# Optimization experiments

Hardware: AMD Instinct MI355X
Metric: run time of the kernel (lower is better)

Reference implementation:

```python
import jax, jax.numpy as jnp
import numpy as np

E = 100000          # number of edges
IN_FEATS = 256      # in_edge_feats
HIDDEN = 128        # hidden_size
K = 16              # neighbors per edge (uniform-degree rendering of ragged lists)


def setup_inputs() -> dict:
    key = jax.random.key(0)
    k1, k2, k3, k4 = jax.random.split(key, 4)
    edge_feats = jax.random.normal(k1, (E, IN_FEATS), dtype=jnp.float32)
    neighbors = jax.random.randint(k2, (E, K), 0, E, dtype=jnp.int32)
    # Linear params (torch Linear: y = x @ W^T + b; here W stored as [in, out])
    W = jax.random.normal(k3, (IN_FEATS, HIDDEN), dtype=jnp.float32) / np.sqrt(IN_FEATS)
    b = jax.random.normal(k4, (HIDDEN,), dtype=jnp.float32) * 0.01
    return {"edge_feats": edge_feats, "neighbors": neighbors, "W": W, "b": b}


def reference(edge_feats, neighbors, W, b):
    # Dense linear transform of all edge features: [E, H]
    t = edge_feats @ W + b
    # Gather each edge's K neighbor transformed features and sum: [E, K, H] -> [E, H]
    nbr_sum = jnp.take(t, neighbors, axis=0).sum(axis=1)
    # agg[i] = t[i] + sum_{n in neighbors[i]} t[n]
    return t + nbr_sum
```

## Files before the change

kernel.cpp:

```cpp
#include <hip/hip_runtime.h>
#include <hip/hip_bf16.h>
#include <stdint.h>

#define E_EDGES 100000
#define IN_F    256
#define HID     128
#define KNB     16
#define NCHUNK  ((E_EDGES + 63) / 64)
#define GEMM_GRID 512

typedef short bf16x8 __attribute__((ext_vector_type(8)));
typedef float f32x4  __attribute__((ext_vector_type(4)));

__device__ __forceinline__ unsigned short f2bf(float f) {
    union { float f; unsigned u; } v; v.f = f;
    unsigned u = v.u;
    u += 0x7fffu + ((u >> 16) & 1u);
    return (unsigned short)(u >> 16);
}

__global__ void conv_w_kernel(const float* __restrict__ W, unsigned short* __restrict__ Wtf) {
    int d = blockIdx.x * 256 + threadIdx.x;
    int f = d >> 6, L = d & 63;
    int k0 = f >> 3, ct = f & 7, quad = L >> 4, l15 = L & 15;
    int n  = ct * 16 + l15;
    int kb = (k0 * 4 + quad) * 8;
    const float* wp = W + (size_t)kb * HID + n;
    unsigned short h[8];
    #pragma unroll
    for (int j = 0; j < 8; ++j) h[j] = f2bf(wp[(size_t)j * HID]);
    uint4 o;
    o.x = (unsigned)h[0] | ((unsigned)h[1] << 16);
    o.y = (unsigned)h[2] | ((unsigned)h[3] << 16);
    o.z = (unsigned)h[4] | ((unsigned)h[5] << 16);
    o.w = (unsigned)h[6] | ((unsigned)h[7] << 16);
    *(uint4*)(Wtf + (size_t)d * 8) = o;
}

__launch_bounds__(256, 2)
__global__ void gemm_t_kernel(const float* __restrict__ A,
                              const unsigned short* __restrict__ Wtf,
                              const float* __restrict__ bias,
                              unsigned short* __restrict__ T) {
    __shared__ unsigned short Bs[32768];
    const int tid  = threadIdx.x;
    const int wave = tid >> 6;
    const int lane = tid & 63;
    const int l15  = lane & 15;
    const int quad = lane >> 4;

    #pragma unroll
    for (int it = 0; it < 16; ++it) {
        int d = it * 256 + tid;
        *(uint4*)(Bs + (size_t)d * 8) = *(const uint4*)(Wtf + (size_t)d * 8);
    }

    float bv[8];
    #pragma unroll
    for (int ct = 0; ct < 8; ++ct) bv[ct] = bias[ct * 16 + l15];

    __syncthreads();

    for (int c = blockIdx.x; c < NCHUNK; c += GEMM_GRID) {
        const int rowbase = c * 64 + wave * 16;
        int arow = rowbase + l15;
        if (arow >= E_EDGES) arow = E_EDGES - 1;

        const float* ap = A + (size_t)arow * IN_F + quad * 8;
        float4 af32[16];
        #pragma unroll
        for (int k0 = 0; k0 < 8; ++k0) {
            af32[2 * k0]     = *(const float4*)(ap + k0 * 32);
            af32[2 * k0 + 1] = *(const float4*)(ap + k0 * 32 + 4);
        }

        bf16x8 apre[8];
        #pragma unroll
        for (int k0 = 0; k0 < 8; ++k0) {
            float4 lo = af32[2 * k0], hi = af32[2 * k0 + 1];
            bf16x8 f;
            f[0] = (short)f2bf(lo.x); f[1] = (short)f2bf(lo.y);
            f[2] = (short)f2bf(lo.z); f[3] = (short)f2bf(lo.w);
            f[4] = (short)f2bf(hi.x); f[5] = (short)f2bf(hi.y);
            f[6] = (short)f2bf(hi.z); f[7] = (short)f2bf(hi.w);
            apre[k0] = f;
        }

        f32x4 acc[8] = {};
        #pragma unroll
        for (int k0 = 0; k0 < 8; ++k0) {
            #pragma unroll
            for (int ct = 0; ct < 8; ++ct) {
                bf16x8 bf = *(const bf16x8*)(Bs + ((size_t)((k0 * 8 + ct) * 64 + lane)) * 8);
                acc[ct] = __builtin_amdgcn_mfma_f32_16x16x32_bf16(apre[k0], bf, acc[ct], 0, 0, 0);
            }
        }

        #pragma unroll
        for (int ct = 0; ct < 8; ++ct) {
            const int col = ct * 16 + l15;
            #pragma unroll
            for (int i = 0; i < 4; ++i) {
                const int row = rowbase + quad * 4 + i;
                if (row < E_EDGES)
                    T[(size_t)row * HID + col] = f2bf(acc[ct][i] + bv[ct]);
            }
        }
    }
}

__launch_bounds__(256)
__global__ void gather_sum_kernel(const unsigned short* __restrict__ T,
                                  const int* __restrict__ nbr,
                                  float* __restrict__ out) {
    __shared__ int sidx[256];
    const int tid   = threadIdx.x;
    const int edge0 = blockIdx.x * 16;
    sidx[tid] = nbr[(size_t)edge0 * KNB + tid];
    __syncthreads();

    const int el   = tid >> 4;
    const int lane = tid & 15;
    const int edge = edge0 + el;

    const unsigned short* tb = T + (size_t)lane * 8;
    uint4 v[17];
    v[0] = *(const uint4*)(tb + (size_t)edge * HID);
    #pragma unroll
    for (int k = 0; k < KNB; ++k)
        v[k + 1] = *(const uint4*)(tb + (size_t)sidx[el * KNB + k] * HID);
    __builtin_amdgcn_sched_barrier(0);

    float acc[8] = {};
    #pragma unroll
    for (int k = 0; k < 17; ++k) {
        unsigned w[4] = { v[k].x, v[k].y, v[k].z, v[k].w };
        union { unsigned u; float f; } c;
        #pragma unroll
        for (int j = 0; j < 4; ++j) {
            c.u = w[j] << 16;          acc[2 * j]     += c.f;
            c.u = w[j] & 0xffff0000u;  acc[2 * j + 1] += c.f;
        }
    }

    float* op = out + (size_t)edge * HID + lane * 8;
    float4 o0 = { acc[0], acc[1], acc[2], acc[3] };
    float4 o1 = { acc[4], acc[5], acc[6], acc[7] };
    *(float4*)op       = o0;
    *(float4*)(op + 4) = o1;
}

extern "C" void kernel_launch(void* const* d_in, const int* in_sizes, int n_in,
                              void* d_out, int out_size, void* d_ws, size_t ws_size,
                              hipStream_t stream) {
    const float* edge_feats = (const float*)d_in[0];
    const int*   neighbors  = (const int*)d_in[1];
    const float* W          = (const float*)d_in[2];
    const float* b          = (const float*)d_in[3];
    float*       out        = (float*)d_out;

    unsigned short* Wtf = (unsigned short*)d_ws;
    unsigned short* T   = (unsigned short*)d_ws + (size_t)IN_F * HID;

    conv_w_kernel<<<16, 256, 0, stream>>>(W, Wtf);
    gemm_t_kernel<<<GEMM_GRID, 256, 0, stream>>>(edge_feats, Wtf, b, T);
    gather_sum_kernel<<<E_EDGES / 16, 256, 0, stream>>>(T, neighbors, out);
}
```

Baseline: 263.4 us.

## Prefetch next A chunk and transpose MFMA to vectorize T stores

Result: faster. 231.7 us (-12.0%).

```diff
diff --git a/kernel.cpp b/kernel.cpp
--- a/kernel.cpp
+++ b/kernel.cpp
@@ -49,31 +49,31 @@
     const int l15  = lane & 15;
     const int quad = lane >> 4;
 
+    int c = blockIdx.x;
+    int arow = c * 64 + wave * 16 + l15;
+    if (arow >= E_EDGES) arow = E_EDGES - 1;
+    const float* ap = A + (size_t)arow * IN_F + quad * 8;
+    float4 af32[16];
+    #pragma unroll
+    for (int k0 = 0; k0 < 8; ++k0) {
+        af32[2 * k0]     = *(const float4*)(ap + k0 * 32);
+        af32[2 * k0 + 1] = *(const float4*)(ap + k0 * 32 + 4);
+    }
+
     #pragma unroll
     for (int it = 0; it < 16; ++it) {
         int d = it * 256 + tid;
         *(uint4*)(Bs + (size_t)d * 8) = *(const uint4*)(Wtf + (size_t)d * 8);
     }
 
-    float bv[8];
+    float4 bv4[8];
     #pragma unroll
-    for (int ct = 0; ct < 8; ++ct) bv[ct] = bias[ct * 16 + l15];
+    for (int ct = 0; ct < 8; ++ct)
+        bv4[ct] = *(const float4*)(bias + ct * 16 + quad * 4);
 
     __syncthreads();
 
-    for (int c = blockIdx.x; c < NCHUNK; c += GEMM_GRID) {
-        const int rowbase = c * 64 + wave * 16;
-        int arow = rowbase + l15;
-        if (arow >= E_EDGES) arow = E_EDGES - 1;
-
-        const float* ap = A + (size_t)arow * IN_F + quad * 8;
-        float4 af32[16];
-        #pragma unroll
-        for (int k0 = 0; k0 < 8; ++k0) {
-            af32[2 * k0]     = *(const float4*)(ap + k0 * 32);
-            af32[2 * k0 + 1] = *(const float4*)(ap + k0 * 32 + 4);
-        }
-
+    for (; c < NCHUNK; c += GEMM_GRID) {
         bf16x8 apre[8];
         #pragma unroll
         for (int k0 = 0; k0 < 8; ++k0) {
@@ -86,24 +86,42 @@
             apre[k0] = f;
         }
 
+        {
+            int cn = c + GEMM_GRID;
+            int arow2 = cn * 64 + wave * 16 + l15;
+            if (arow2 >= E_EDGES) arow2 = E_EDGES - 1;
+            const float* ap2 = A + (size_t)arow2 * IN_F + quad * 8;
+            #pragma unroll
+            for (int k0 = 0; k0 < 8; ++k0) {
+                af32[2 * k0]     = *(const float4*)(ap2 + k0 * 32);
+                af32[2 * k0 + 1] = *(const float4*)(ap2 + k0 * 32 + 4);
+            }
+        }
+        __builtin_amdgcn_sched_barrier(0);
+
         f32x4 acc[8] = {};
         #pragma unroll
         for (int k0 = 0; k0 < 8; ++k0) {
             #pragma unroll
             for (int ct = 0; ct < 8; ++ct) {
                 bf16x8 bf = *(const bf16x8*)(Bs + ((size_t)((k0 * 8 + ct) * 64 + lane)) * 8);
-                acc[ct] = __builtin_amdgcn_mfma_f32_16x16x32_bf16(apre[k0], bf, acc[ct], 0, 0, 0);
+                acc[ct] = __builtin_amdgcn_mfma_f32_16x16x32_bf16(bf, apre[k0], acc[ct], 0, 0, 0);
             }
         }
 
-        #pragma unroll
-        for (int ct = 0; ct < 8; ++ct) {
-            const int col = ct * 16 + l15;
+        const int row = c * 64 + wave * 16 + l15;
+        if (row < E_EDGES) {
+            unsigned short* tp = T + (size_t)row * HID + quad * 4;
             #pragma unroll
-            for (int i = 0; i < 4; ++i) {
-                const int row = rowbase + quad * 4 + i;
-                if (row < E_EDGES)
-                    T[(size_t)row * HID + col] = f2bf(acc[ct][i] + bv[ct]);
+            for (int ct = 0; ct < 8; ++ct) {
+                unsigned short h0 = f2bf(acc[ct][0] + bv4[ct].x);
+                unsigned short h1 = f2bf(acc[ct][1] + bv4[ct].y);
+                unsigned short h2 = f2bf(acc[ct][2] + bv4[ct].z);
+                unsigned short h3 = f2bf(acc[ct][3] + bv4[ct].w);
+                uint2 o;
+                o.x = (unsigned)h0 | ((unsigned)h1 << 16);
+                o.y = (unsigned)h2 | ((unsigned)h3 << 16);
+                *(uint2*)(tp + ct * 16) = o;
             }
         }
     }
```
